# Kernel tuning notes

Measured on AMD Instinct MI355X. Metric: run time of the kernel, lower is better.

Reference implementation:

```python
import jax, jax.numpy as jnp
import numpy as np

N = 50000          # nodes
DEG = 16           # in-degree per node
E = N * DEG        # edges
HID = 128          # hidden_channels (x_channels)
NH = 32            # num_heads (hardcoded in StarPool)
HD = HID // NH     # head dim
ECH = 64           # edge channels = num_rbf + num_edge_attr
NG = 64            # number of graphs in batch
OUT = 1            # output_dim
EPS = 1e-5


def setup_inputs() -> dict:
    key = jax.random.key(0)
    ks = jax.random.split(key, 12)
    x = jax.random.normal(ks[0], (N, HID), jnp.float32)
    edge_attr = jax.random.normal(ks[1], (E, ECH), jnp.float32)
    # edge_index: row0 = source j (random), row1 = target i covering all nodes
    src = jax.random.randint(ks[2], (E,), 0, N, dtype=jnp.int32)
    dst = jnp.repeat(jnp.arange(N, dtype=jnp.int32), DEG)
    edge_index = jnp.stack([src, dst], axis=0)
    batch = jnp.sort(jax.random.randint(ks[3], (N,), 0, NG, dtype=jnp.int32))
    # learned parameters (xavier-ish scaling)
    s_h = 1.0 / np.sqrt(HID)
    s_e = 1.0 / np.sqrt(ECH)
    Wq = jax.random.normal(ks[4], (HID, HID), jnp.float32) * s_h
    bq = jnp.zeros((HID,), jnp.float32)
    Wkv = jax.random.normal(ks[5], (HID, HID), jnp.float32) * s_h
    bkv = jnp.zeros((HID,), jnp.float32)
    Wdk = jax.random.normal(ks[6], (ECH, HID), jnp.float32) * s_e
    bdk = jnp.zeros((HID,), jnp.float32)
    ln_in_g = jnp.ones((HID,), jnp.float32)
    ln_in_b = jnp.zeros((HID,), jnp.float32)
    ln_out_g = jnp.ones((HID,), jnp.float32)
    ln_out_b = jnp.zeros((HID,), jnp.float32)
    Wout = jax.random.normal(ks[7], (HID, OUT), jnp.float32) * s_h
    bout = jnp.zeros((OUT,), jnp.float32)
    return {"x": x, "edge_attr": edge_attr, "Wq": Wq, "bq": bq, "Wkv": Wkv,
            "bkv": bkv, "Wdk": Wdk, "bdk": bdk, "ln_in_g": ln_in_g,
            "ln_in_b": ln_in_b, "ln_out_g": ln_out_g, "ln_out_b": ln_out_b,
            "Wout": Wout, "bout": bout, "edge_index": edge_index, "batch": batch}


def _layernorm(z, g, b):
    m = jnp.mean(z, axis=-1, keepdims=True)
    v = jnp.mean(jnp.square(z - m), axis=-1, keepdims=True)
    return (z - m) * jax.lax.rsqrt(v + EPS) * g + b


def reference(x, edge_attr, Wq, bq, Wkv, bkv, Wdk, bdk,
              ln_in_g, ln_in_b, ln_out_g, ln_out_b, Wout, bout,
              edge_index, batch):
    n = x.shape[0]
    residue = x
    xn = _layernorm(x, ln_in_g, ln_in_b)
    q = (xn @ Wq + bq).reshape(n, NH, HD)
    k = (xn @ Wkv + bkv).reshape(n, NH, HD)          # v = k in StarPool
    dk = (edge_attr @ Wdk + bdk).reshape(-1, NH, HD)
    src, dst = edge_index[0], edge_index[1]          # j (source), i (target)
    k_j = k[src]                                     # [E, NH, HD]
    attn = jax.nn.silu(jnp.sum(q[dst] * k_j * dk, axis=-1))  # [E, NH]
    msg = k_j * attn[:, :, None]                     # [E, NH, HD]
    # scatter-mean over target nodes
    counts = jax.ops.segment_sum(jnp.ones((msg.shape[0],), x.dtype), dst, num_segments=n)
    agg = jax.ops.segment_sum(msg, dst, num_segments=n)
    agg = agg / jnp.clip(counts, 1.0)[:, None, None]
    h = residue + agg.reshape(n, HID)
    # perm = unique(edge_index[1]) == arange(n) by input construction (identity)
    h = residue + _layernorm(h, ln_out_g, ln_out_b)  # dropout p=0 -> identity
    # per-graph mean readout (reduce_op='mean')
    gcnt = jax.ops.segment_sum(jnp.ones((n,), x.dtype), batch, num_segments=NG)
    g = jax.ops.segment_sum(h, batch, num_segments=NG) / jnp.clip(gcnt, 1.0)[:, None]
    # output MLP with 'pass' (identity) activation
    return g @ Wout + bout
```

## Files before the change

### kernel.cpp

```cpp
#include <hip/hip_runtime.h>
#include <hip/hip_bf16.h>

#define N_NODES 50000
#define DEG 16
#define NE 800000
#define HID 128
#define NH 32
#define ECH 64
#define NG 64
#define NSLOT 32
#define LN_EPS 1e-5f

typedef __bf16 bf16x8 __attribute__((ext_vector_type(8)));
typedef float f32x4 __attribute__((ext_vector_type(4)));

__device__ __forceinline__ unsigned short f2bf(float f) {
  unsigned int u = __float_as_uint(f);
  u += 0x7FFFu + ((u >> 16) & 1u);
  return (unsigned short)(u >> 16);
}
__device__ __forceinline__ unsigned int pack2(float a, float b) {
  return (unsigned int)f2bf(a) | ((unsigned int)f2bf(b) << 16);
}

__global__ void prep_kernel(const float* __restrict__ Wq, const float* __restrict__ Wkv,
                            const float* __restrict__ Wdk,
                            unsigned short* __restrict__ WBf,
                            unsigned short* __restrict__ Wdkf,
                            float* __restrict__ gsum) {
  int b = blockIdx.x, t = threadIdx.x;
  if (b < 16) {
    int n = b;
    for (int idx = t; idx < 2048; idx += 256) {
      int j = idx & 7, l = (idx >> 3) & 63, kk = idx >> 9;
      int col = n * 16 + (l & 15);
      int k = kk * 32 + (l >> 4) * 8 + j;
      float v = (col < HID) ? Wq[k * HID + col] : Wkv[k * HID + (col - HID)];
      WBf[((n * 4 + kk) * 64 + l) * 8 + j] = f2bf(v);
    }
  } else if (b < 24) {
    int n2 = b - 16;
    for (int idx = t; idx < 1024; idx += 256) {
      int j = idx & 7, l = (idx >> 3) & 63, kk = idx >> 9;
      int col = n2 * 16 + (l & 15);
      int k = kk * 32 + (l >> 4) * 8 + j;
      Wdkf[((n2 * 2 + kk) * 64 + l) * 8 + j] = f2bf(Wdk[k * HID + col]);
    }
  } else {
    int chunk = b - 24;
    const int tot = NG * NSLOT * HID / 8;
    for (int i = chunk * tot + t; i < (chunk + 1) * tot; i += 256)
      gsum[i] = 0.0f;
  }
}

__global__ __launch_bounds__(256) void node_kernel(
    const float* __restrict__ x, const float* __restrict__ bq,
    const float* __restrict__ bkv, const float* __restrict__ lng,
    const float* __restrict__ lnb, const unsigned short* __restrict__ WBf,
    float* __restrict__ qout, unsigned short* __restrict__ kout) {
  __shared__ __align__(16) unsigned short xn[64 * HID];
  int t = threadIdx.x;
  int node0 = blockIdx.x * 64;
  {
    int row = t >> 2, q4 = t & 3;
    int c0 = q4 * 32;
    int node = node0 + row;
    float v[32];
    if (node < N_NODES) {
      const float4* xp = (const float4*)(x + node * HID + c0);
#pragma unroll
      for (int i = 0; i < 8; i++) {
        float4 f = xp[i];
        v[4 * i] = f.x; v[4 * i + 1] = f.y; v[4 * i + 2] = f.z; v[4 * i + 3] = f.w;
      }
    } else {
#pragma unroll
      for (int i = 0; i < 32; i++) v[i] = 0.f;
    }
    float s = 0.f;
#pragma unroll
    for (int i = 0; i < 32; i++) s += v[i];
    s += __shfl_xor(s, 1); s += __shfl_xor(s, 2);
    float m = s * (1.0f / HID);
    float sq = 0.f;
#pragma unroll
    for (int i = 0; i < 32; i++) { float d = v[i] - m; sq += d * d; }
    sq += __shfl_xor(sq, 1); sq += __shfl_xor(sq, 2);
    float rstd = rsqrtf(sq * (1.0f / HID) + LN_EPS);
#pragma unroll
    for (int ch = 0; ch < 4; ch++) {
      float w0[8];
#pragma unroll
      for (int j = 0; j < 8; j++) {
        int c = c0 + ch * 8 + j;
        w0[j] = (v[ch * 8 + j] - m) * rstd * lng[c] + lnb[c];
      }
      uint4 u;
      u.x = pack2(w0[0], w0[1]); u.y = pack2(w0[2], w0[3]);
      u.z = pack2(w0[4], w0[5]); u.w = pack2(w0[6], w0[7]);
      int byte = row * 256 + ((c0 * 2 + ch * 16) ^ ((row & 7) << 4));
      *(uint4*)((char*)xn + byte) = u;
    }
  }
  __syncthreads();
  int w = t >> 6, l = t & 63;
  int arow = w * 16 + (l & 15);
  bf16x8 a[4];
#pragma unroll
  for (int kk = 0; kk < 4; kk++) {
    int byte = arow * 256 + ((kk * 64 + (l >> 4) * 16) ^ ((arow & 7) << 4));
    a[kk] = *(const bf16x8*)((const char*)xn + byte);
  }
  f32x4 acc[16];
#pragma unroll
  for (int n = 0; n < 16; n++) acc[n] = (f32x4){0.f, 0.f, 0.f, 0.f};
#pragma unroll
  for (int n = 0; n < 16; n++)
#pragma unroll
    for (int kk = 0; kk < 4; kk++) {
      bf16x8 bfr = *(const bf16x8*)(WBf + ((n * 4 + kk) * 64 + l) * 8);
      acc[n] = __builtin_amdgcn_mfma_f32_16x16x32_bf16(a[kk], bfr, acc[n], 0, 0, 0);
    }
#pragma unroll
  for (int n = 0; n < 16; n++) {
    int col = n * 16 + (l & 15);
    float bias = (col < HID) ? bq[col] : bkv[col - HID];
#pragma unroll
    for (int r = 0; r < 4; r++) {
      int node = node0 + w * 16 + (l >> 4) * 4 + r;
      if (node < N_NODES) {
        float vv = acc[n][r] + bias;
        if (col < HID) qout[node * HID + col] = vv;
        else kout[node * HID + (col - HID)] = f2bf(vv);
      }
    }
  }
}

__global__ __launch_bounds__(256, 2) void edge_kernel(
    const float* __restrict__ x, const float* __restrict__ ea,
    const int* __restrict__ src_arr, const int* __restrict__ batch,
    const float* __restrict__ bdk, const float* __restrict__ lng,
    const float* __restrict__ lnb, const float* __restrict__ qg,
    const unsigned short* __restrict__ kbf,
    const unsigned short* __restrict__ Wdkf, float* __restrict__ gsum) {
  __shared__ __align__(16) unsigned short wdk_s[8 * 2 * 64 * 8];
  __shared__ __align__(16) float xq_s[8 * HID];
  __shared__ __align__(16) float prm_s[3 * HID];
  __shared__ __align__(16) float at_s[4 * 16 * 33];
  __shared__ __align__(16) float h_s[4 * 132];
  __shared__ int src_s[64];
  __shared__ int b4[4];
  int t = threadIdx.x;
  int node0 = blockIdx.x * 4;
  int w = t >> 6, l = t & 63, el = l & 15, eh = l >> 4;
  int ni = node0 + w;
  size_t e0n = (size_t)ni * DEG;

  xq_s[t]       = x[(size_t)node0 * HID + t];
  xq_s[256 + t] = x[(size_t)node0 * HID + 256 + t];
  xq_s[512 + t] = qg[(size_t)node0 * HID + t];
  xq_s[768 + t] = qg[(size_t)node0 * HID + 256 + t];
  if (t < HID) { prm_s[t] = bdk[t]; prm_s[HID + t] = lng[t]; prm_s[2 * HID + t] = lnb[t]; }
#pragma unroll
  for (int i = 0; i < 4; i++) {
    int idx = (i * 256 + t) * 8;
    *(uint4*)(wdk_s + idx) = *(const uint4*)(Wdkf + idx);
  }
  if (t < 64) src_s[t] = src_arr[(size_t)node0 * DEG + t];
  if (t < 4) b4[t] = batch[node0 + t];

  int srcn = src_arr[e0n + el];
  const float* earow = ea + (e0n + el) * ECH + eh * 8;
  float4 ea00 = *(const float4*)(earow);
  float4 ea01 = *(const float4*)(earow + 4);
  float4 ea10 = *(const float4*)(earow + 32);
  float4 ea11 = *(const float4*)(earow + 36);
  const unsigned short* kr = kbf + (size_t)srcn * HID;
  uint2 kg[8];
#pragma unroll
  for (int n = 0; n < 8; n++) kg[n] = *(const uint2*)(kr + n * 16 + eh * 4);

  bf16x8 bfr[2];
  bfr[0][0] = (__bf16)ea00.x; bfr[0][1] = (__bf16)ea00.y;
  bfr[0][2] = (__bf16)ea00.z; bfr[0][3] = (__bf16)ea00.w;
  bfr[0][4] = (__bf16)ea01.x; bfr[0][5] = (__bf16)ea01.y;
  bfr[0][6] = (__bf16)ea01.z; bfr[0][7] = (__bf16)ea01.w;
  bfr[1][0] = (__bf16)ea10.x; bfr[1][1] = (__bf16)ea10.y;
  bfr[1][2] = (__bf16)ea10.z; bfr[1][3] = (__bf16)ea10.w;
  bfr[1][4] = (__bf16)ea11.x; bfr[1][5] = (__bf16)ea11.y;
  bfr[1][6] = (__bf16)ea11.z; bfr[1][7] = (__bf16)ea11.w;

  __syncthreads();

  unsigned int kw[16];
#pragma unroll
  for (int e = 0; e < 16; e++) {
    int sw = src_s[w * 16 + e];
    kw[e] = *(const unsigned int*)(kbf + (size_t)sw * HID + 2 * l);
  }

  f32x4 acc[8];
#pragma unroll
  for (int n = 0; n < 8; n++) acc[n] = (f32x4){0.f, 0.f, 0.f, 0.f};
#pragma unroll
  for (int n = 0; n < 8; n++)
#pragma unroll
    for (int kk = 0; kk < 2; kk++) {
      bf16x8 af = *(const bf16x8*)(wdk_s + ((n * 2 + kk) * 64 + l) * 8);
      acc[n] = __builtin_amdgcn_mfma_f32_16x16x32_bf16(af, bfr[kk], acc[n], 0, 0, 0);
    }

#pragma unroll
  for (int n = 0; n < 8; n++) {
    const int cb = n * 16 + eh * 4;
    f32x4 qv = *(const f32x4*)&xq_s[512 + w * HID + cb];
    f32x4 bd = *(const f32x4*)&prm_s[cb];
    float k0 = __uint_as_float(kg[n].x << 16);
    float k1 = __uint_as_float(kg[n].x & 0xFFFF0000u);
    float k2 = __uint_as_float(kg[n].y << 16);
    float k3 = __uint_as_float(kg[n].y & 0xFFFF0000u);
    float d0 = acc[n][0] + bd[0];
    float d1 = acc[n][1] + bd[1];
    float d2 = acc[n][2] + bd[2];
    float d3 = acc[n][3] + bd[3];
    float s = qv[0] * k0 * d0 + qv[1] * k1 * d1 + qv[2] * k2 * d2 + qv[3] * k3 * d3;
    float at = s * __builtin_amdgcn_rcpf(1.0f + __expf(-s));
    at_s[w * 528 + el * 33 + n * 4 + eh] = at;
  }

  int hl = l >> 1;
  float macc0 = 0.f, macc1 = 0.f;
#pragma unroll
  for (int e = 0; e < 16; e++) {
    float at = at_s[w * 528 + e * 33 + hl];
    float k0 = __uint_as_float(kw[e] << 16);
    float k1 = __uint_as_float(kw[e] & 0xFFFF0000u);
    macc0 = fmaf(k0, at, macc0);
    macc1 = fmaf(k1, at, macc1);
  }
  float2 xv = *(const float2*)&xq_s[w * HID + 2 * l];
  float h10 = xv.x + macc0 * 0.0625f;
  float h11 = xv.y + macc1 * 0.0625f;
  float ss = h10 + h11;
  ss += __shfl_xor(ss, 1);  ss += __shfl_xor(ss, 2);  ss += __shfl_xor(ss, 4);
  ss += __shfl_xor(ss, 8);  ss += __shfl_xor(ss, 16); ss += __shfl_xor(ss, 32);
  float mean = ss * (1.0f / HID);
  float dv0 = h10 - mean, dv1 = h11 - mean;
  float vv = dv0 * dv0 + dv1 * dv1;
  vv += __shfl_xor(vv, 1);  vv += __shfl_xor(vv, 2);  vv += __shfl_xor(vv, 4);
  vv += __shfl_xor(vv, 8);  vv += __shfl_xor(vv, 16); vv += __shfl_xor(vv, 32);
  float rstd = rsqrtf(vv * (1.0f / HID) + LN_EPS);
  float2 gv = *(const float2*)&prm_s[HID + 2 * l];
  float2 bv = *(const float2*)&prm_s[2 * HID + 2 * l];
  float2 ho;
  ho.x = xv.x + dv0 * rstd * gv.x + bv.x;
  ho.y = xv.y + dv1 * rstd * gv.y + bv.y;
  *(float2*)&h_s[w * 132 + 2 * l] = ho;
  __syncthreads();
  if (t < HID) {
    int c = t;
    int slot = blockIdx.x & (NSLOT - 1);
    float accu = h_s[c];
#pragma unroll
    for (int nn = 1; nn < 4; nn++) {
      if (b4[nn] == b4[nn - 1]) accu += h_s[nn * 132 + c];
      else {
        atomicAdd(&gsum[(b4[nn - 1] * NSLOT + slot) * HID + c], accu);
        accu = h_s[nn * 132 + c];
      }
    }
    atomicAdd(&gsum[(b4[3] * NSLOT + slot) * HID + c], accu);
  }
}

__global__ void readout_kernel(const float* __restrict__ gsum,
                               const int* __restrict__ batch,
                               const float* __restrict__ Wout,
                               const float* __restrict__ bout,
                               float* __restrict__ out) {
  int g = blockIdx.x, l = threadIdx.x;
  int lo = 0, hi = N_NODES;
  while (lo < hi) { int mid = (lo + hi) >> 1; if (batch[mid] < g) lo = mid + 1; else hi = mid; }
  int lo2 = lo, hi2 = N_NODES;
  while (lo2 < hi2) { int mid = (lo2 + hi2) >> 1; if (batch[mid] < g + 1) lo2 = mid + 1; else hi2 = mid; }
  int cnt = lo2 - lo; if (cnt < 1) cnt = 1;
  float a0 = 0.f, a1 = 0.f;
#pragma unroll 4
  for (int s = 0; s < NSLOT; s++) {
    const float* row = gsum + ((size_t)g * NSLOT + s) * HID;
    a0 += row[l];
    a1 += row[64 + l];
  }
  float v = a0 * Wout[l] + a1 * Wout[64 + l];
#pragma unroll
  for (int s = 32; s >= 1; s >>= 1) v += __shfl_xor(v, s);
  if (l == 0) out[g] = v / (float)cnt + bout[0];
}

extern "C" void kernel_launch(void* const* d_in, const int* in_sizes, int n_in,
                              void* d_out, int out_size, void* d_ws, size_t ws_size,
                              hipStream_t stream) {
  const float* x         = (const float*)d_in[0];
  const float* edge_attr = (const float*)d_in[1];
  const float* Wq        = (const float*)d_in[2];
  const float* bq        = (const float*)d_in[3];
  const float* Wkv       = (const float*)d_in[4];
  const float* bkv       = (const float*)d_in[5];
  const float* Wdk       = (const float*)d_in[6];
  const float* bdk       = (const float*)d_in[7];
  const float* ln_in_g   = (const float*)d_in[8];
  const float* ln_in_b   = (const float*)d_in[9];
  const float* ln_out_g  = (const float*)d_in[10];
  const float* ln_out_b  = (const float*)d_in[11];
  const float* Wout      = (const float*)d_in[12];
  const float* bout      = (const float*)d_in[13];
  const int* edge_index  = (const int*)d_in[14];
  const int* batch       = (const int*)d_in[15];
  float* outp = (float*)d_out;

  char* ws = (char*)d_ws;
  float* qbuf          = (float*)ws;
  unsigned short* kbuf = (unsigned short*)(ws + 25600000);
  unsigned short* WBf  = (unsigned short*)(ws + 25600000 + 12800000);
  unsigned short* Wdkf = (unsigned short*)(ws + 25600000 + 12800000 + 65536);
  float* gsum          = (float*)(ws + 25600000 + 12800000 + 65536 + 16384);

  prep_kernel<<<32, 256, 0, stream>>>(Wq, Wkv, Wdk, WBf, Wdkf, gsum);
  node_kernel<<<(N_NODES + 63) / 64, 256, 0, stream>>>(x, bq, bkv, ln_in_g, ln_in_b,
                                                       WBf, qbuf, kbuf);
  edge_kernel<<<N_NODES / 4, 256, 0, stream>>>(x, edge_attr, edge_index, batch, bdk,
                                               ln_out_g, ln_out_b, qbuf, kbuf, Wdkf, gsum);
  readout_kernel<<<NG, 64, 0, stream>>>(gsum, batch, Wout, bout, outp);
}
```

Baseline: 144.8 us.

## Stage gathered K rows in swizzled LDS, drop Wdk LDS copy, raise occupancy

After: 135.3 us. 1.07x faster.

```diff
diff --git a/kernel.cpp b/kernel.cpp
--- a/kernel.cpp
+++ b/kernel.cpp
@@ -138,59 +138,48 @@
   }
 }
 
-__global__ __launch_bounds__(256, 2) void edge_kernel(
+__global__ __launch_bounds__(256, 4) void edge_kernel(
     const float* __restrict__ x, const float* __restrict__ ea,
     const int* __restrict__ src_arr, const int* __restrict__ batch,
     const float* __restrict__ bdk, const float* __restrict__ lng,
     const float* __restrict__ lnb, const float* __restrict__ qg,
     const unsigned short* __restrict__ kbf,
     const unsigned short* __restrict__ Wdkf, float* __restrict__ gsum) {
-  __shared__ __align__(16) unsigned short wdk_s[8 * 2 * 64 * 8];
   __shared__ __align__(16) float xq_s[8 * HID];
   __shared__ __align__(16) float prm_s[3 * HID];
   __shared__ __align__(16) float at_s[4 * 16 * 33];
   __shared__ __align__(16) float h_s[4 * 132];
+  __shared__ __align__(16) unsigned short k_s[4 * 16 * HID];
   __shared__ int src_s[64];
   __shared__ int b4[4];
   int t = threadIdx.x;
   int node0 = blockIdx.x * 4;
   int w = t >> 6, l = t & 63, el = l & 15, eh = l >> 4;
-  int ni = node0 + w;
-  size_t e0n = (size_t)ni * DEG;
+  size_t e0n = (size_t)(node0 + w) * DEG;
 
   xq_s[t]       = x[(size_t)node0 * HID + t];
   xq_s[256 + t] = x[(size_t)node0 * HID + 256 + t];
   xq_s[512 + t] = qg[(size_t)node0 * HID + t];
   xq_s[768 + t] = qg[(size_t)node0 * HID + 256 + t];
   if (t < HID) { prm_s[t] = bdk[t]; prm_s[HID + t] = lng[t]; prm_s[2 * HID + t] = lnb[t]; }
-#pragma unroll
-  for (int i = 0; i < 4; i++) {
-    int idx = (i * 256 + t) * 8;
-    *(uint4*)(wdk_s + idx) = *(const uint4*)(Wdkf + idx);
-  }
   if (t < 64) src_s[t] = src_arr[(size_t)node0 * DEG + t];
   if (t < 4) b4[t] = batch[node0 + t];
 
-  int srcn = src_arr[e0n + el];
   const float* earow = ea + (e0n + el) * ECH + eh * 8;
-  float4 ea00 = *(const float4*)(earow);
-  float4 ea01 = *(const float4*)(earow + 4);
-  float4 ea10 = *(const float4*)(earow + 32);
-  float4 ea11 = *(const float4*)(earow + 36);
-  const unsigned short* kr = kbf + (size_t)srcn * HID;
-  uint2 kg[8];
-#pragma unroll
-  for (int n = 0; n < 8; n++) kg[n] = *(const uint2*)(kr + n * 16 + eh * 4);
+  f32x4 ea00 = __builtin_nontemporal_load((const f32x4*)(earow));
+  f32x4 ea01 = __builtin_nontemporal_load((const f32x4*)(earow + 4));
+  f32x4 ea10 = __builtin_nontemporal_load((const f32x4*)(earow + 32));
+  f32x4 ea11 = __builtin_nontemporal_load((const f32x4*)(earow + 36));
 
   bf16x8 bfr[2];
-  bfr[0][0] = (__bf16)ea00.x; bfr[0][1] = (__bf16)ea00.y;
-  bfr[0][2] = (__bf16)ea00.z; bfr[0][3] = (__bf16)ea00.w;
-  bfr[0][4] = (__bf16)ea01.x; bfr[0][5] = (__bf16)ea01.y;
-  bfr[0][6] = (__bf16)ea01.z; bfr[0][7] = (__bf16)ea01.w;
-  bfr[1][0] = (__bf16)ea10.x; bfr[1][1] = (__bf16)ea10.y;
-  bfr[1][2] = (__bf16)ea10.z; bfr[1][3] = (__bf16)ea10.w;
-  bfr[1][4] = (__bf16)ea11.x; bfr[1][5] = (__bf16)ea11.y;
-  bfr[1][6] = (__bf16)ea11.z; bfr[1][7] = (__bf16)ea11.w;
+  bfr[0][0] = (__bf16)ea00[0]; bfr[0][1] = (__bf16)ea00[1];
+  bfr[0][2] = (__bf16)ea00[2]; bfr[0][3] = (__bf16)ea00[3];
+  bfr[0][4] = (__bf16)ea01[0]; bfr[0][5] = (__bf16)ea01[1];
+  bfr[0][6] = (__bf16)ea01[2]; bfr[0][7] = (__bf16)ea01[3];
+  bfr[1][0] = (__bf16)ea10[0]; bfr[1][1] = (__bf16)ea10[1];
+  bfr[1][2] = (__bf16)ea10[2]; bfr[1][3] = (__bf16)ea10[3];
+  bfr[1][4] = (__bf16)ea11[0]; bfr[1][5] = (__bf16)ea11[1];
+  bfr[1][6] = (__bf16)ea11[2]; bfr[1][7] = (__bf16)ea11[3];
 
   __syncthreads();
 
@@ -200,6 +189,10 @@
     int sw = src_s[w * 16 + e];
     kw[e] = *(const unsigned int*)(kbf + (size_t)sw * HID + 2 * l);
   }
+  char* kswW = (char*)k_s + w * 4096;
+#pragma unroll
+  for (int e = 0; e < 16; e++)
+    *(unsigned int*)(kswW + e * 256 + ((4 * l) ^ ((e & 7) << 4))) = kw[e];
 
   f32x4 acc[8];
 #pragma unroll
@@ -208,19 +201,21 @@
   for (int n = 0; n < 8; n++)
 #pragma unroll
     for (int kk = 0; kk < 2; kk++) {
-      bf16x8 af = *(const bf16x8*)(wdk_s + ((n * 2 + kk) * 64 + l) * 8);
+      bf16x8 af = *(const bf16x8*)(Wdkf + ((n * 2 + kk) * 64 + l) * 8);
       acc[n] = __builtin_amdgcn_mfma_f32_16x16x32_bf16(af, bfr[kk], acc[n], 0, 0, 0);
     }
 
+  const char* kswR = (const char*)k_s + w * 4096;
 #pragma unroll
   for (int n = 0; n < 8; n++) {
     const int cb = n * 16 + eh * 4;
     f32x4 qv = *(const f32x4*)&xq_s[512 + w * HID + cb];
     f32x4 bd = *(const f32x4*)&prm_s[cb];
-    float k0 = __uint_as_float(kg[n].x << 16);
-    float k1 = __uint_as_float(kg[n].x & 0xFFFF0000u);
-    float k2 = __uint_as_float(kg[n].y << 16);
-    float k3 = __uint_as_float(kg[n].y & 0xFFFF0000u);
+    uint2 kk2 = *(const uint2*)(kswR + el * 256 + ((n * 32 + eh * 8) ^ ((el & 7) << 4)));
+    float k0 = __uint_as_float(kk2.x << 16);
+    float k1 = __uint_as_float(kk2.x & 0xFFFF0000u);
+    float k2 = __uint_as_float(kk2.y << 16);
+    float k3 = __uint_as_float(kk2.y & 0xFFFF0000u);
     float d0 = acc[n][0] + bd[0];
     float d1 = acc[n][1] + bd[1];
     float d2 = acc[n][2] + bd[2];
```
